# Kernel tuning notes

Hardware: AMD Instinct MI355X
Metric: run time of the kernel (lower is better)

Reference implementation:

```python
import jax, jax.numpy as jnp
import numpy as np

DIM = 1024
NUM_HEADS = 8  # only used for the scale; heads are never actually split
SCALE = float((DIM // NUM_HEADS) ** 0.5)


def _attn(x, wq, wk, wv):
    # Single-head full-dim attention, faithful to the source (no head split).
    Q = x @ wq.T  # [B,S,D]
    K = x @ wk.T
    V = x @ wv.T
    scores = jnp.einsum('bqd,bkd->bqk', Q, K) / SCALE  # [B,S,S]
    attn = jax.nn.softmax(scores, axis=-1)
    return jnp.einsum('bqk,bkd->bqd', attn, V)


def setup_inputs() -> dict:
    key = jax.random.key(0)
    ks = jax.random.split(key, 9)
    B, S, D = 4, 2048, DIM
    w = lambda k: jax.random.normal(k, (D, D), dtype=jnp.float32) * 0.02
    return {
        'x': jax.random.normal(ks[0], (B, S, D), dtype=jnp.float32),
        'wq1': w(ks[1]), 'wk1': w(ks[2]), 'wv1': w(ks[3]),
        'fc1_w': w(ks[4]),
        'wq2': w(ks[5]), 'wk2': w(ks[6]), 'wv2': w(ks[7]),
        'fc2_w': w(ks[8]),
    }


def reference(x, wq1, wk1, wv1, fc1_w, wq2, wk2, wv2, fc2_w):
    h = _attn(x, wq1, wk1, wv1)
    h = jax.nn.silu(h)
    h = h @ fc1_w.T
    h = _attn(h, wq2, wk2, wv2)
    h = jax.nn.silu(h)
    h = h @ fc2_w.T
    return jax.nn.softmax(h, axis=-1)
```

## Files before the change

kernel.cpp:

```cpp
#include <hip/hip_runtime.h>
#include <math.h>


typedef __attribute__((ext_vector_type(8))) int i32x8;
typedef __attribute__((ext_vector_type(4))) int i32x4;
typedef __attribute__((ext_vector_type(4))) float f32x4;
typedef unsigned char u8;
typedef unsigned int u32;

#define EPI_F8 1
#define EPI_QKV 2
#define EPI_EXP 3
#define EPI_PV 4
#define EPI_EXPF32 5

__device__ __forceinline__ void gload_lds16(const void* g, void* l) {
    __builtin_amdgcn_global_load_lds(
        (const __attribute__((address_space(1))) void*)g,
        (__attribute__((address_space(3))) void*)l, 16, 0, 0);
}

__device__ __forceinline__ u8 cvt_f8(float v) {
    return (u8)(__builtin_amdgcn_cvt_pk_fp8_f32(v, v, 0, false) & 0xFF);
}

__device__ __forceinline__ u32 pack_f8x4(float v0, float v1, float v2, float v3) {
    int p01 = __builtin_amdgcn_cvt_pk_fp8_f32(v0, v1, 0, false);
    int p23 = __builtin_amdgcn_cvt_pk_fp8_f32(v2, v3, 0, false);
    return (u32)(p01 & 0xFFFF) | ((u32)p23 << 16);
}

template <int EPI>
__global__ __launch_bounds__(256) void gemm_fp8(
    const u8* __restrict__ A, const u8* __restrict__ B,
    void* __restrict__ C0, void* __restrict__ C1, void* __restrict__ C2,
    int K, int ldA, int ldB, int ldC,
    long long bsA, long long bsB, long long bsC, float alpha, float beta)
{
    __shared__ u8 sA[128 * 128];
    __shared__ u8 sB[128 * 128];

    const int tid = threadIdx.x;
    const int wave = tid >> 6, lane = tid & 63;
    const int wm = wave >> 1, wn = wave & 1;
    const int m0 = blockIdx.y * 128, n0 = blockIdx.x * 128;
    const long long z = blockIdx.z;

    const u8* pA = A + z * bsA;
    const u8* pB = B + z * bsB;

    int blkid[4], rs_[4], cs16[4];
#pragma unroll
    for (int i = 0; i < 4; i++) {
        blkid[i] = wave * 256 + i * 64 + lane;
        rs_[i] = blkid[i] >> 3;
        cs16[i] = ((blkid[i] & 7) ^ (rs_[i] & 7)) * 16;
    }

    f32x4 acc[4][4] = {};
    const int fr = lane & 15, fc2 = (lane >> 4) * 2;

    for (int k0 = 0; k0 < K; k0 += 128) {
#pragma unroll
        for (int i = 0; i < 4; i++) {
            gload_lds16(pA + (long long)(m0 + rs_[i]) * ldA + k0 + cs16[i],
                        sA + blkid[i] * 16);
            gload_lds16(pB + (long long)(n0 + rs_[i]) * ldB + k0 + cs16[i],
                        sB + blkid[i] * 16);
        }
        __syncthreads();

        i32x8 a[4], b[4];
#pragma unroll
        for (int i = 0; i < 4; i++) {
            const int row = wm * 64 + i * 16 + fr;
            const int sw = row & 7;
            i32x4 lo = *(const i32x4*)(sA + row * 128 + ((fc2 + 0) ^ sw) * 16);
            i32x4 hi = *(const i32x4*)(sA + row * 128 + ((fc2 + 1) ^ sw) * 16);
            a[i] = __builtin_shufflevector(lo, hi, 0, 1, 2, 3, 4, 5, 6, 7);
        }
#pragma unroll
        for (int j = 0; j < 4; j++) {
            const int row = wn * 64 + j * 16 + fr;
            const int sw = row & 7;
            i32x4 lo = *(const i32x4*)(sB + row * 128 + ((fc2 + 0) ^ sw) * 16);
            i32x4 hi = *(const i32x4*)(sB + row * 128 + ((fc2 + 1) ^ sw) * 16);
            b[j] = __builtin_shufflevector(lo, hi, 0, 1, 2, 3, 4, 5, 6, 7);
        }
#pragma unroll
        for (int i = 0; i < 4; i++)
#pragma unroll
            for (int j = 0; j < 4; j++)
                acc[i][j] = __builtin_amdgcn_mfma_scale_f32_16x16x128_f8f6f4(
                    a[i], b[j], acc[i][j], 0 , 0 ,
                    0, 0x7F7F7F7F, 0, 0x7F7F7F7F);
        __syncthreads();
    }

    const int col = lane & 15;
    const int rbase = (lane >> 4) * 4;

    if (EPI == EPI_EXP) {
        u8* P = (u8*)C0 + z * bsC;
        float* rsum = (float*)C1 + z * 2048;
#pragma unroll
        for (int j = 0; j < 4; j++) {
            const int Cq = n0 + wn * 64 + j * 16 + col;
            float part = 0.f;
#pragma unroll
            for (int i = 0; i < 4; i++) {
                const int R0 = m0 + wm * 64 + i * 16 + rbase;
                float e0 = __expf(acc[i][j][0] * alpha);
                float e1 = __expf(acc[i][j][1] * alpha);
                float e2 = __expf(acc[i][j][2] * alpha);
                float e3 = __expf(acc[i][j][3] * alpha);
                part += (e0 + e1) + (e2 + e3);
                *(u32*)(P + (long long)Cq * ldC + R0) =
                    pack_f8x4(e0 * 0.0625f, e1 * 0.0625f,
                              e2 * 0.0625f, e3 * 0.0625f);
            }
            part += __shfl_xor(part, 16);
            part += __shfl_xor(part, 32);
            if (lane < 16) atomicAdd(&rsum[Cq], part);
        }
        return;
    }

    if (EPI == EPI_EXPF32) {
        float* Cw = (float*)C0;
        float* rsum = (float*)C1;
#pragma unroll
        for (int j = 0; j < 4; j++) {
            const int Cq = n0 + wn * 64 + j * 16 + col;
            float part = 0.f;
#pragma unroll
            for (int i = 0; i < 4; i++) {
                const int R0 = m0 + wm * 64 + i * 16 + rbase;
                float4 e;
                e.x = __expf(acc[i][j][0] * alpha);
                e.y = __expf(acc[i][j][1] * alpha);
                e.z = __expf(acc[i][j][2] * alpha);
                e.w = __expf(acc[i][j][3] * alpha);
                part += (e.x + e.y) + (e.z + e.w);
                *(float4*)(Cw + (long long)Cq * ldC + R0) = e;
            }
            part += __shfl_xor(part, 16);
            part += __shfl_xor(part, 32);
            if (lane < 16) atomicAdd(&rsum[Cq], part);
        }
        return;
    }

#pragma unroll
    for (int j = 0; j < 4; j++) {
        const int Cq = n0 + wn * 64 + j * 16 + col;
        float inv;
        if (EPI == EPI_PV) {
            const float* rsum = (const float*)C1 + z * 2048;
            inv = alpha / rsum[Cq];
        }
#pragma unroll
        for (int i = 0; i < 4; i++) {
            const int R0 = m0 + wm * 64 + i * 16 + rbase;
            if (EPI == EPI_F8) {
                u8* C = (u8*)C0 + z * bsC;
                *(u32*)(C + (long long)Cq * ldC + R0) =
                    pack_f8x4(acc[i][j][0] * alpha, acc[i][j][1] * alpha,
                              acc[i][j][2] * alpha, acc[i][j][3] * alpha);
            } else if (EPI == EPI_PV) {
                u8* C = (u8*)C0 + z * bsC;
                float v[4];
#pragma unroll
                for (int r = 0; r < 4; r++) {
                    float t = acc[i][j][r] * inv;
                    v[r] = (t / (1.f + __expf(-t))) * beta;
                }
                *(u32*)(C + (long long)Cq * ldC + R0) =
                    pack_f8x4(v[0], v[1], v[2], v[3]);
            } else {
                const int seg = R0 >> 10;
                const int db = R0 & 1023;
                if (seg == 2) {
                    const int bb = Cq >> 11, tt = Cq & 2047;
                    u8* VTp = (u8*)C2;
#pragma unroll
                    for (int r = 0; r < 4; r++)
                        VTp[(long long)bb * (1024LL * 2048) +
                            (long long)(db + r) * 2048 + tt] =
                            cvt_f8(acc[i][j][r] * alpha);
                } else {
                    u8* C = seg ? (u8*)C1 : (u8*)C0;
                    *(u32*)(C + (long long)Cq * 1024 + db) =
                        pack_f8x4(acc[i][j][0] * alpha, acc[i][j][1] * alpha,
                                  acc[i][j][2] * alpha, acc[i][j][3] * alpha);
                }
            }
        }
    }
}

__global__ __launch_bounds__(256) void convert_all(
    const float* x, const float* w0, const float* w1, const float* w2,
    const float* w3, const float* w4, const float* w5, const float* w6,
    const float* w7, u8* __restrict__ ax, u8* __restrict__ wf,
    float* __restrict__ rz)
{
    const int bid = blockIdx.x;
    if (bid < 24) {
        float4 zero = {0.f, 0.f, 0.f, 0.f};
        *(float4*)(rz + ((long long)bid * 256 + threadIdx.x) * 4) = zero;
    }
    const float* src;
    u8* dst;
    float scale;
    long long i;
    if (bid < 8192) {
        src = x; dst = ax; scale = 8.f;
        i = ((long long)bid * 256 + threadIdx.x) * 4;
    } else {
        const float* ws[8] = {w0, w1, w2, w3, w4, w5, w6, w7};
        const int wi = (bid - 8192) >> 10;
        src = ws[wi]; scale = 256.f;
        dst = wf + (long long)wi * 1024 * 1024;
        i = (((long long)(bid - 8192) & 1023) * 256 + threadIdx.x) * 4;
    }
    float4 v = *(const float4*)(src + i);
    *(u32*)(dst + i) = pack_f8x4(v.x * scale, v.y * scale,
                                 v.z * scale, v.w * scale);
}

__global__ __launch_bounds__(256) void normalize_1024(
    const float* __restrict__ e, const float* __restrict__ rsum,
    float* __restrict__ out)
{
    const long long row = blockIdx.x;
    const float inv = 1.0f / rsum[row];
    const float* p = e + row * 1024;
    float* o = out + row * 1024;
    float4 v = *(const float4*)(p + threadIdx.x * 4);
    float4 ov;
    ov.x = v.x * inv; ov.y = v.y * inv; ov.z = v.z * inv; ov.w = v.w * inv;
    *(float4*)(o + threadIdx.x * 4) = ov;
}

extern "C" void kernel_launch(void* const* d_in, const int* in_sizes, int n_in,
                              void* d_out, int out_size, void* d_ws, size_t ws_size,
                              hipStream_t stream)
{
    float* out = (float*)d_out;

    constexpr int Bt = 4, S = 2048, D = 1024;
    constexpr int M = Bt * S;
    const long long MD = (long long)M * D;
    const long long DD = (long long)D * D;
    const long long SD = (long long)S * D;
    const long long SS = (long long)S * S;

    u8* Af = (u8*)d_ws;
    u8* Wf = Af + MD;
    u8* Qf = Wf + 8 * DD;
    u8* Kf = Qf + MD;
    u8* VT = Kf + MD;
    u8* Pf = VT + MD;
    u8* Hs = Pf + (long long)Bt * SS;
    float* SC = (float*)(Hs + MD);
    float* rsum0 = SC + MD;
    float* rsum1 = rsum0 + M;
    float* rsum2 = rsum1 + M;

    const dim3 blk(256);

    const float SOFT = 0.08838834764831845f;
    const float a_qkv[2] = {8.f / 2048.f, 1024.f / 65536.f};
    const float a_qk[2]  = {SOFT / 64.f, SOFT / 1048576.f};
    const float a_pv[2]  = {2.0f, 1.f / 64.f};
    const float b_pv[2]  = {256.f, 65536.f};
    const float a_fc[2]  = {256.f / 65536.f, 1.f / 16777216.f};

    convert_all<<<dim3(16384), blk, 0, stream>>>(
        (const float*)d_in[0], (const float*)d_in[1], (const float*)d_in[2],
        (const float*)d_in[3], (const float*)d_in[4], (const float*)d_in[5],
        (const float*)d_in[6], (const float*)d_in[7], (const float*)d_in[8],
        Af, Wf, rsum0);

    const dim3 gqkv(M / 128, 3 * D / 128, 1);
    const dim3 gqk(S / 128, S / 128, Bt);
    const dim3 gpv(S / 128, D / 128, Bt);
    const dim3 gw(M / 128, D / 128, 1);

    for (int layer = 0; layer < 2; layer++) {
        const u8* wqkv = Wf + (long long)(layer * 4) * DD;
        const u8* fc   = Wf + (long long)(layer * 4 + 3) * DD;
        float* rsum    = layer ? rsum1 : rsum0;

        gemm_fp8<EPI_QKV><<<gqkv, blk, 0, stream>>>(
            wqkv, Af, Qf, Kf, VT, D, D, D, D, 0, 0, 0, a_qkv[layer], 0.f);
        gemm_fp8<EPI_EXP><<<gqk, blk, 0, stream>>>(
            Kf, Qf, Pf, rsum, nullptr, D, D, D, S, SD, SD, SS,
            a_qk[layer], 0.f);
        gemm_fp8<EPI_PV><<<gpv, blk, 0, stream>>>(
            VT, Pf, Hs, rsum, nullptr, S, S, S, D,
            (long long)D * S, SS, SD, a_pv[layer], b_pv[layer]);
        if (layer == 0) {
            gemm_fp8<EPI_F8><<<gw, blk, 0, stream>>>(
                fc, Hs, Af, nullptr, nullptr, D, D, D, D, 0, 0, 0,
                a_fc[0], 0.f);
        } else {
            gemm_fp8<EPI_EXPF32><<<gw, blk, 0, stream>>>(
                fc, Hs, SC, rsum2, nullptr, D, D, D, D, 0, 0, 0,
                a_fc[1], 0.f);
        }
    }

    normalize_1024<<<dim3(M), blk, 0, stream>>>(SC, rsum2, out);
}
```

Baseline: 344.5 us.

## Fold Wq^T Wk into a precomputed matrix to drop the K projection

Rewrites the scores as x·(Wq^T Wk)·x^T. A small weight-only GEMM first builds Wq^T·Wk for each layer, with Wq and Wk transposed to fp8 by a new kernel. The per-layer projection GEMM then produces only R = x·(WqᵀWk)ᵀ and V, shrinking its N dimension from 3D to 2D, and the QK GEMM reads the fp8 activations directly as the K operand. This costs a fused-weight GEMM per call and an extra fp8 rounding of the product matrix, with new scale constants that may affect accuracy.

```diff
diff --git a/kernel.cpp b/kernel.cpp
--- a/kernel.cpp
+++ b/kernel.cpp
@@ -9,7 +9,7 @@
 typedef unsigned int u32;
 
 #define EPI_F8 1
-#define EPI_QKV 2
+#define EPI_RV 2
 #define EPI_EXP 3
 #define EPI_PV 4
 #define EPI_EXPF32 5
@@ -180,16 +180,16 @@
             } else {
                 const int seg = R0 >> 10;
                 const int db = R0 & 1023;
-                if (seg == 2) {
+                if (seg == 1) {
                     const int bb = Cq >> 11, tt = Cq & 2047;
                     u8* VTp = (u8*)C2;
 #pragma unroll
                     for (int r = 0; r < 4; r++)
                         VTp[(long long)bb * (1024LL * 2048) +
                             (long long)(db + r) * 2048 + tt] =
-                            cvt_f8(acc[i][j][r] * alpha);
+                            cvt_f8(acc[i][j][r] * beta);
                 } else {
-                    u8* C = seg ? (u8*)C1 : (u8*)C0;
+                    u8* C = (u8*)C0;
                     *(u32*)(C + (long long)Cq * 1024 + db) =
                         pack_f8x4(acc[i][j][0] * alpha, acc[i][j][1] * alpha,
                                   acc[i][j][2] * alpha, acc[i][j][3] * alpha);
@@ -200,10 +200,9 @@
 }
 
 __global__ __launch_bounds__(256) void convert_all(
-    const float* x, const float* w0, const float* w1, const float* w2,
-    const float* w3, const float* w4, const float* w5, const float* w6,
-    const float* w7, u8* __restrict__ ax, u8* __restrict__ wf,
-    float* __restrict__ rz)
+    const float* x, const float* wv1, const float* wv2, const float* fc1,
+    const float* fc2, u8* __restrict__ ax, u8* __restrict__ bproj,
+    u8* __restrict__ wfc, float* __restrict__ rz)
 {
     const int bid = blockIdx.x;
     if (bid < 24) {
@@ -218,15 +217,38 @@
         src = x; dst = ax; scale = 8.f;
         i = ((long long)bid * 256 + threadIdx.x) * 4;
     } else {
-        const float* ws[8] = {w0, w1, w2, w3, w4, w5, w6, w7};
-        const int wi = (bid - 8192) >> 10;
-        src = ws[wi]; scale = 256.f;
-        dst = wf + (long long)wi * 1024 * 1024;
-        i = (((long long)(bid - 8192) & 1023) * 256 + threadIdx.x) * 4;
+        const int idx = bid - 8192;
+        const int wi = idx >> 10;
+        const float* srcs[4] = {wv1, wv2, fc1, fc2};
+        u8* dsts[4] = {bproj + (1 << 20), bproj + 3 * (1 << 20),
+                       wfc, wfc + (1 << 20)};
+        src = srcs[wi]; dst = dsts[wi]; scale = 256.f;
+        i = (((long long)(idx & 1023)) * 256 + threadIdx.x) * 4;
     }
     float4 v = *(const float4*)(src + i);
     *(u32*)(dst + i) = pack_f8x4(v.x * scale, v.y * scale,
                                  v.z * scale, v.w * scale);
+}
+
+__global__ __launch_bounds__(256) void convert_t(
+    const float* wq1, const float* wk1, const float* wq2, const float* wk2,
+    u8* __restrict__ o)
+{
+    const float* srcs[4] = {wq1, wk1, wq2, wk2};
+    const float* src = srcs[blockIdx.y];
+    u8* dst = o + (long long)blockIdx.y * (1 << 20);
+    const int q0 = (blockIdx.x & 15) * 64, d0 = (blockIdx.x >> 4) * 64;
+    const int qq = (threadIdx.x & 15) * 4, dd = (threadIdx.x >> 4) * 4;
+    float4 v[4];
+#pragma unroll
+    for (int s = 0; s < 4; s++)
+        v[s] = *(const float4*)(src + (long long)(q0 + qq + s) * 1024 + d0 + dd);
+    const float* vf = (const float*)v;
+#pragma unroll
+    for (int r = 0; r < 4; r++)
+        *(u32*)(dst + (long long)(d0 + dd + r) * 1024 + q0 + qq) =
+            pack_f8x4(vf[0 * 4 + r] * 256.f, vf[1 * 4 + r] * 256.f,
+                      vf[2 * 4 + r] * 256.f, vf[3 * 4 + r] * 256.f);
 }
 
 __global__ __launch_bounds__(256) void normalize_1024(
@@ -257,10 +279,11 @@
     const long long SS = (long long)S * S;
 
     u8* Af = (u8*)d_ws;
-    u8* Wf = Af + MD;
-    u8* Qf = Wf + 8 * DD;
-    u8* Kf = Qf + MD;
-    u8* VT = Kf + MD;
+    u8* Bproj = Af + MD;
+    u8* WqT = Bproj + 2 * 2048 * 1024;
+    u8* Wfc = WqT + 4 * DD;
+    u8* Rf = Wfc + 2 * DD;
+    u8* VT = Rf + MD;
     u8* Pf = VT + MD;
     u8* Hs = Pf + (long long)Bt * SS;
     float* SC = (float*)(Hs + MD);
@@ -271,32 +294,39 @@
     const dim3 blk(256);
 
     const float SOFT = 0.08838834764831845f;
-    const float a_qkv[2] = {8.f / 2048.f, 1024.f / 65536.f};
-    const float a_qk[2]  = {SOFT / 64.f, SOFT / 1048576.f};
-    const float a_pv[2]  = {2.0f, 1.f / 64.f};
-    const float b_pv[2]  = {256.f, 65536.f};
-    const float a_fc[2]  = {256.f / 65536.f, 1.f / 16777216.f};
-
-    convert_all<<<dim3(16384), blk, 0, stream>>>(
-        (const float*)d_in[0], (const float*)d_in[1], (const float*)d_in[2],
-        (const float*)d_in[3], (const float*)d_in[4], (const float*)d_in[5],
-        (const float*)d_in[6], (const float*)d_in[7], (const float*)d_in[8],
-        Af, Wf, rsum0);
-
-    const dim3 gqkv(M / 128, 3 * D / 128, 1);
+    const float a_d1   = 1.f / 64.f;
+    const float a_R[2] = {1.f / 512.f, 1.f / 1024.f};
+    const float b_V[2] = {1.f / 256.f, 1.f / 64.f};
+    const float a_qk[2] = {SOFT / 128.f, SOFT / 65536.f};
+    const float a_pv[2] = {2.0f, 1.f / 64.f};
+    const float b_pv[2] = {256.f, 65536.f};
+    const float a_fc[2] = {256.f / 65536.f, 1.f / 16777216.f};
+
+    convert_all<<<dim3(12288), blk, 0, stream>>>(
+        (const float*)d_in[0], (const float*)d_in[3], (const float*)d_in[7],
+        (const float*)d_in[4], (const float*)d_in[8], Af, Bproj, Wfc, rsum0);
+    convert_t<<<dim3(256, 4), blk, 0, stream>>>(
+        (const float*)d_in[1], (const float*)d_in[2], (const float*)d_in[5],
+        (const float*)d_in[6], WqT);
+    gemm_fp8<EPI_F8><<<dim3(8, 8, 2), blk, 0, stream>>>(
+        WqT, WqT + DD, Bproj, nullptr, nullptr, D, D, D, D,
+        2 * DD, 2 * DD, (long long)2048 * 1024, a_d1, 0.f);
+
+    const dim3 grv(M / 128, 2048 / 128, 1);
     const dim3 gqk(S / 128, S / 128, Bt);
     const dim3 gpv(S / 128, D / 128, Bt);
     const dim3 gw(M / 128, D / 128, 1);
 
     for (int layer = 0; layer < 2; layer++) {
-        const u8* wqkv = Wf + (long long)(layer * 4) * DD;
-        const u8* fc   = Wf + (long long)(layer * 4 + 3) * DD;
-        float* rsum    = layer ? rsum1 : rsum0;
-
-        gemm_fp8<EPI_QKV><<<gqkv, blk, 0, stream>>>(
-            wqkv, Af, Qf, Kf, VT, D, D, D, D, 0, 0, 0, a_qkv[layer], 0.f);
+        const u8* bp = Bproj + (long long)layer * 2048 * 1024;
+        const u8* fc = Wfc + (long long)layer * DD;
+        float* rsum = layer ? rsum1 : rsum0;
+
+        gemm_fp8<EPI_RV><<<grv, blk, 0, stream>>>(
+            bp, Af, Rf, nullptr, VT, D, D, D, D, 0, 0, 0,
+            a_R[layer], b_V[layer]);
         gemm_fp8<EPI_EXP><<<gqk, blk, 0, stream>>>(
-            Kf, Qf, Pf, rsum, nullptr, D, D, D, S, SD, SD, SS,
+            Af, Rf, Pf, rsum, nullptr, D, D, D, S, SD, SD, SS,
             a_qk[layer], 0.f);
         gemm_fp8<EPI_PV><<<gpv, blk, 0, stream>>>(
             VT, Pf, Hs, rsum, nullptr, S, S, S, D,
```

Measured after the change: 336.6 us. -2.3%, faster.
